# Kernel tuning notes

Hardware: AMD Instinct MI355X
Metric: run time of the kernel (lower is better)

## Reference

```python
import jax, jax.numpy as jnp
import numpy as np

D_MODEL = 1024
D_K = 64
D_V = 64
N_HEADS = 16
LN_EPS = 1e-5


def setup_inputs() -> dict:
    key = jax.random.key(0)
    ks = jax.random.split(key, 9)
    B, S = 2, 2048
    scale = 0.02
    return {
        "input_Q": jax.random.normal(ks[0], (B, S, D_MODEL), dtype=jnp.float32),
        "input_K": jax.random.normal(ks[1], (B, S, D_MODEL), dtype=jnp.float32),
        "input_V": jax.random.normal(ks[2], (B, S, D_MODEL), dtype=jnp.float32),
        "W_Q": jax.random.normal(ks[3], (D_MODEL, N_HEADS * D_K), dtype=jnp.float32) * scale,
        "W_K": jax.random.normal(ks[4], (D_MODEL, N_HEADS * D_K), dtype=jnp.float32) * scale,
        "W_V": jax.random.normal(ks[5], (D_MODEL, N_HEADS * D_V), dtype=jnp.float32) * scale,
        "W_O": jax.random.normal(ks[6], (N_HEADS * D_V, D_MODEL), dtype=jnp.float32) * scale,
        "ln_gamma": jnp.ones((D_MODEL,), dtype=jnp.float32),
        "ln_beta": jnp.zeros((D_MODEL,), dtype=jnp.float32),
    }


def reference(input_Q, input_K, input_V, W_Q, W_K, W_V, W_O, ln_gamma, ln_beta):
    B, Lq, _ = input_Q.shape
    Lk = input_K.shape[1]
    # projections -> [B, H, L, d]
    Q = (input_Q @ W_Q).reshape(B, Lq, N_HEADS, D_K).transpose(0, 2, 1, 3)
    K = (input_K @ W_K).reshape(B, Lk, N_HEADS, D_K).transpose(0, 2, 1, 3)
    V = (input_V @ W_V).reshape(B, Lk, N_HEADS, D_V).transpose(0, 2, 1, 3)
    # scores: [B, H, Lq, Lk]
    scores = jnp.einsum("bhqd,bhkd->bhqk", Q, K) / jnp.sqrt(jnp.float32(D_K))
    # NOTE: source uses nn.Softmax(dim=1) -> softmax over the HEADS axis (faithful quirk)
    attn = jax.nn.softmax(scores, axis=1)
    context = jnp.einsum("bhqk,bhkv->bhqv", attn, V)
    context = context.transpose(0, 2, 1, 3).reshape(B, Lq, N_HEADS * D_V)
    output = context @ W_O
    # residual + LayerNorm over last dim
    x = output + input_Q
    mu = jnp.mean(x, axis=-1, keepdims=True)
    var = jnp.mean(jnp.square(x - mu), axis=-1, keepdims=True)
    return (x - mu) / jnp.sqrt(var + LN_EPS) * ln_gamma + ln_beta
```

## Files before the change

### kernel.cpp

```cpp
#include <hip/hip_runtime.h>
#include <cstdint>
#include <cstddef>

#define DM 1024
#define HEADS 16
#define DHEAD 64
#define SEQ 2048
#define BATCH 2

typedef __bf16 bf16x8 __attribute__((ext_vector_type(8)));
typedef float  f32x4  __attribute__((ext_vector_type(4)));
typedef unsigned short u16;
typedef unsigned int u32;
typedef u16 u16x8 __attribute__((ext_vector_type(8)));
typedef u16 u16x4 __attribute__((ext_vector_type(4)));

__device__ __forceinline__ float bf2f(u16 u){
    union { u32 i; float f; } v; v.i = ((u32)u) << 16; return v.f;
}
__device__ __forceinline__ u16 f2bf(float f){
    union { float f; u32 i; } v; v.f = f;
    u32 r = v.i + 0x7FFF + ((v.i >> 16) & 1);
    return (u16)(r >> 16);
}
__device__ __forceinline__ u16 f2bf_rhu(float f){
    union { float f; u32 i; } v; v.f = f;
    return (u16)((v.i + 0x8000u) >> 16);
}
__device__ __forceinline__ float fexp2(float x){
    float r;
    asm volatile("v_exp_f32 %0, %1\n\ts_nop 1" : "=v"(r) : "v"(x));
    return r;
}
__device__ __forceinline__ void gload16(const u16* g, u16* l){
    __builtin_amdgcn_global_load_lds(
        (const __attribute__((address_space(1))) u32*)g,
        (__attribute__((address_space(3))) u32*)l, 16, 0, 0);
}
__device__ __forceinline__ int probe_flag(const u16* q){
    int cnt = 0;
    #pragma unroll
    for (int i = 0; i < 32; i += 2){
        int e = (q[i] >> 7) & 0xFF;
        if (e >= 90 && e <= 141) cnt++;
    }
    return (cnt >= 12) ? 1 : 0;
}

__global__ __launch_bounds__(256) void k_cvt3(const void* __restrict__ s0,
                                              const void* __restrict__ s1,
                                              const void* __restrict__ s2,
                                              u16* __restrict__ dstbase,
                                              int* __restrict__ hdr, int n){
    int isbf = probe_flag((const u16*)s0);
    if (blockIdx.x == 0 && blockIdx.y == 0 && threadIdx.x == 0){
        hdr[0] = isbf;
        #pragma unroll
        for (int c = 1; c <= 24; c++) hdr[c] = 0;
    }
    int z = blockIdx.y;
    const void* src = (z == 0) ? s0 : ((z == 1) ? s1 : s2);
    u16* dst = dstbase + (size_t)z * n;
    int i = (blockIdx.x * 256 + threadIdx.x) * 8;
    if (i >= n) return;
    if (isbf){
        *(u16x8*)&dst[i] = *(const u16x8*)((const u16*)src + i);
    } else {
        const float* s = (const float*)src + i;
        u16x8 o;
        #pragma unroll
        for (int j = 0; j < 8; j++) o[j] = f2bf(s[j]);
        *(u16x8*)&dst[i] = o;
    }
}

__global__ void k_tcvt4(const void* __restrict__ w0, const void* __restrict__ w1,
                        const void* __restrict__ w2, const void* __restrict__ w3,
                        u16* __restrict__ dstbase,
                        const int* __restrict__ flag, int R, int C){
    __shared__ u16 tile[32][33];
    int z = blockIdx.z;
    const void* src = (z == 0) ? w0 : ((z == 1) ? w1 : ((z == 2) ? w2 : w3));
    u16* dst = dstbase + (size_t)z * R * C;
    bool isbf = (*flag != 0);
    int c0 = blockIdx.x * 32, r0 = blockIdx.y * 32;
    int tx = threadIdx.x, ty = threadIdx.y;
    #pragma unroll
    for (int i = 0; i < 32; i += 8){
        size_t idx = (size_t)(r0 + ty + i) * C + c0 + tx;
        tile[ty + i][tx] = isbf ? ((const u16*)src)[idx] : f2bf(((const float*)src)[idx]);
    }
    __syncthreads();
    #pragma unroll
    for (int i = 0; i < 32; i += 8)
        dst[(size_t)(c0 + ty + i) * R + r0 + tx] = tile[tx][ty + i];
}

template<int NJ>
__global__ __launch_bounds__(256, 2) void k_gemmT(const u16* __restrict__ A0,
                                                  const u16* __restrict__ Bt0,
                                                  u16* __restrict__ C0,
                                                  size_t strA, size_t strB, size_t strC,
                                                  int M, int N, int K){
    constexpr int BN = NJ * 32;
    __shared__ u16 lsA[128 * 64];
    __shared__ u16 lsB[BN * 64];
    int z = blockIdx.z;
    const u16* A  = A0  + strA * z;
    const u16* Bt = Bt0 + strB * z;
    u16* C = C0 + strC * z;
    int m0 = blockIdx.y * 128, n0 = blockIdx.x * BN;
    int t = threadIdx.x, lane = t & 63, w = t >> 6;
    int l15 = lane & 15, quad = lane >> 4;
    int wm = (w & 1) * 64, wn = (w >> 1) * (NJ * 16);
    f32x4 acc[4][NJ] = {};
    for (int k0 = 0; k0 < K; k0 += 64){
        __syncthreads();
        #pragma unroll
        for (int j = 0; j < 4; j++){
            int ub = j * 256 + w * 64;
            int u  = ub + lane;
            int r  = u >> 3, cg = (u & 7) ^ (r & 7);
            gload16(&A[(size_t)(m0 + r) * K + k0 + cg * 8], &lsA[ub * 8]);
        }
        #pragma unroll
        for (int j = 0; j < NJ; j++){
            int ub = j * 256 + w * 64;
            int u  = ub + lane;
            int r  = u >> 3, cg = (u & 7) ^ (r & 7);
            gload16(&Bt[(size_t)(n0 + r) * K + k0 + cg * 8], &lsB[ub * 8]);
        }
        __syncthreads();
        bf16x8 af[4][2], bfr[NJ][2];
        #pragma unroll
        for (int i = 0; i < 4; i++){
            int row = wm + i * 16 + l15;
            #pragma unroll
            for (int kk = 0; kk < 2; kk++)
                af[i][kk] = *(const bf16x8*)&lsA[row * 64 + (((kk * 4 + quad) ^ (row & 7)) * 8)];
        }
        #pragma unroll
        for (int jj = 0; jj < NJ; jj++){
            int row = wn + jj * 16 + l15;
            #pragma unroll
            for (int kk = 0; kk < 2; kk++)
                bfr[jj][kk] = *(const bf16x8*)&lsB[row * 64 + (((kk * 4 + quad) ^ (row & 7)) * 8)];
        }
        #pragma unroll
        for (int i = 0; i < 4; i++)
            #pragma unroll
            for (int jj = 0; jj < NJ; jj++)
                #pragma unroll
                for (int kk = 0; kk < 2; kk++)
                    acc[i][jj] = __builtin_amdgcn_mfma_f32_16x16x32_bf16(af[i][kk], bfr[jj][kk],
                                                                         acc[i][jj], 0, 0, 0);
    }
    #pragma unroll
    for (int i = 0; i < 4; i++)
        #pragma unroll
        for (int jj = 0; jj < NJ; jj++)
            #pragma unroll
            for (int r = 0; r < 4; r++){
                int m = m0 + wm + i * 16 + quad * 4 + r;
                int n = n0 + wn + jj * 16 + l15;
                C[(size_t)m * N + n] = f2bf(acc[i][jj][r]);
            }
}

__global__ __launch_bounds__(1024, 4) void k_attn5(const u16* __restrict__ Qp,
                                                   const u16* __restrict__ Kp,
                                                   const u16* __restrict__ Vt,
                                                   u16* __restrict__ c0,
                                                   u16* __restrict__ c1,
                                                   u16* __restrict__ c2,
                                                   u16* __restrict__ c3,
                                                   int* __restrict__ cnt,
                                                   int ncomboM1, int iters){
    __shared__ u16 ebuf[2][16][64][36];
    __shared__ int s_combo, s_slot;
    int t = threadIdx.x;
    if (t == 0){
        int xcc;
        asm volatile("s_getreg_b32 %0, hwreg(HW_REG_XCC_ID)" : "=s"(xcc));
        int start = xcc & ncomboM1;
        int combo = -1, slot = -1;
        for (int a = 0; a <= ncomboM1 && combo < 0; a++){
            int c = (start + a) & ncomboM1;
            int s = atomicAdd(&cnt[c], 1);
            if (s < 32){ combo = c; slot = s; }
        }
        s_combo = combo; s_slot = slot;
    }
    __syncthreads();
    int combo = s_combo;
    if (combo < 0) return;
    int b = combo & 1, chunk = combo >> 1;
    int q0 = s_slot * 64;
    int h = t >> 6, lane = t & 63, l15 = lane & 15, quad = lane >> 4;
    u16* outp = (chunk == 0) ? c0 : ((chunk == 1) ? c1 : ((chunk == 2) ? c2 : c3));
    const float cexp = 0.125f * 1.44269504f;
    int kbeg = chunk * (iters << 5);

    bf16x8 qf[4][2];
    #pragma unroll
    for (int sub = 0; sub < 4; sub++)
        #pragma unroll
        for (int ch = 0; ch < 2; ch++)
            qf[sub][ch] = *(const bf16x8*)&Qp[((size_t)(b * SEQ + q0 + sub * 16 + l15)) * DM
                                             + h * DHEAD + ch * 32 + quad * 8];

    f32x4 oacc[4][4] = {};
    int sq = t >> 4, sku = (t & 15) * 2;

    auto score_phase = [&](int it){
        int k0 = kbeg + (it << 5), bf = it & 1;
        #pragma unroll
        for (int kt = 0; kt < 2; kt++){
            const u16* kb = Kp + ((size_t)(b * SEQ + k0 + kt * 16 + l15)) * DM + h * DHEAD + quad * 8;
            bf16x8 kf0 = *(const bf16x8*)(kb);
            bf16x8 kf1 = *(const bf16x8*)(kb + 32);
            #pragma unroll
            for (int sub = 0; sub < 4; sub++){
                f32x4 sc = {};
                sc = __builtin_amdgcn_mfma_f32_16x16x32_bf16(qf[sub][0], kf0, sc, 0, 0, 0);
                sc = __builtin_amdgcn_mfma_f32_16x16x32_bf16(qf[sub][1], kf1, sc, 0, 0, 0);
                #pragma unroll
                for (int r = 0; r < 4; r++)
                    ebuf[bf][h][sub * 16 + quad * 4 + r][kt * 16 + l15] =
                        f2bf_rhu(fexp2(sc[r] * cexp));
            }
        }
    };

    score_phase(0);
    for (int it = 0; it < iters; it++){
        int bf = it & 1;
        __syncthreads();
        {
            u32 ev[16];
            float s0 = 0.f, s1 = 0.f;
            #pragma unroll
            for (int hh = 0; hh < 16; hh++){
                u32 u = *(const u32*)&ebuf[bf][hh][sq][sku];
                ev[hh] = u;
                union { u32 i; float f; } lo, hi;
                lo.i = u << 16; hi.i = u & 0xFFFF0000u;
                s0 += lo.f; s1 += hi.f;
            }
            float r0 = __builtin_amdgcn_rcpf(s0);
            float r1 = __builtin_amdgcn_rcpf(s1);
            #pragma unroll
            for (int hh = 0; hh < 16; hh++){
                union { u32 i; float f; } lo, hi, p0, p1;
                lo.i = ev[hh] << 16; hi.i = ev[hh] & 0xFFFF0000u;
                p0.f = lo.f * r0; p1.f = hi.f * r1;
                *(u32*)&ebuf[bf][hh][sq][sku] =
                    __builtin_amdgcn_perm(p1.i + 0x8000u, p0.i + 0x8000u, 0x07060302u);
            }
        }
        __syncthreads();
        int k0 = kbeg + (it << 5);
        bf16x8 pa[4];
        #pragma unroll
        for (int sub = 0; sub < 4; sub++){
            const u16* pp = &ebuf[bf][h][sub * 16 + l15][quad * 8];
            union { bf16x8 v; u16x4 q[2]; } pu;
            pu.q[0] = *(const u16x4*)pp;
            pu.q[1] = *(const u16x4*)(pp + 4);
            pa[sub] = pu.v;
        }
        #pragma unroll
        for (int vt = 0; vt < 4; vt++){
            bf16x8 vf = *(const bf16x8*)&Vt[((size_t)b * DM + h * DHEAD + vt * 16 + l15) * SEQ
                                            + k0 + quad * 8];
            #pragma unroll
            for (int sub = 0; sub < 4; sub++)
                oacc[sub][vt] = __builtin_amdgcn_mfma_f32_16x16x32_bf16(pa[sub], vf, oacc[sub][vt], 0, 0, 0);
        }
        if (it + 1 < iters) score_phase(it + 1);
    }
    #pragma unroll
    for (int sub = 0; sub < 4; sub++)
        #pragma unroll
        for (int vt = 0; vt < 4; vt++)
            #pragma unroll
            for (int r = 0; r < 4; r++){
                int q = q0 + sub * 16 + quad * 4 + r;
                int n = h * DHEAD + vt * 16 + l15;
                outp[((size_t)b * SEQ + q) * DM + n] = f2bf(oacc[sub][vt][r]);
            }
}

__global__ __launch_bounds__(256) void k_reduce(const u16* __restrict__ a,
                                                const u16* __restrict__ b,
                                                const u16* __restrict__ c,
                                                const u16* __restrict__ d,
                                                u16* __restrict__ dst, int n, int nch){
    int i = (blockIdx.x * 256 + threadIdx.x) * 8;
    if (i >= n) return;
    u16x8 x = *(const u16x8*)&a[i];
    u16x8 y = *(const u16x8*)&b[i];
    u16x8 o;
    if (nch == 4){
        u16x8 zc = *(const u16x8*)&c[i];
        u16x8 zd = *(const u16x8*)&d[i];
        #pragma unroll
        for (int j = 0; j < 8; j++)
            o[j] = f2bf((bf2f(x[j]) + bf2f(y[j])) + (bf2f(zc[j]) + bf2f(zd[j])));
    } else {
        #pragma unroll
        for (int j = 0; j < 8; j++) o[j] = f2bf(bf2f(x[j]) + bf2f(y[j]));
    }
    *(u16x8*)&dst[i] = o;
}

__global__ __launch_bounds__(256) void k_ln(const u16* __restrict__ O,
                                            const void* __restrict__ Qin,
                                            const void* __restrict__ gamma,
                                            const void* __restrict__ beta,
                                            void* __restrict__ out,
                                            const int* __restrict__ flag){
    __shared__ float red[4][2];
    bool isbf = (*flag != 0);
    int row = blockIdx.x;
    int t = threadIdx.x;
    const u16* op = O + (size_t)row * DM;
    float xv[4];
    float s1 = 0.f, s2 = 0.f;
    #pragma unroll
    for (int i = 0; i < 4; i++){
        int idx = i * 256 + t;
        float q = isbf ? bf2f(((const u16*)Qin)[(size_t)row * DM + idx])
                       : ((const float*)Qin)[(size_t)row * DM + idx];
        float x = bf2f(op[idx]) + q;
        xv[i] = x; s1 += x; s2 += x * x;
    }
    #pragma unroll
    for (int off = 32; off; off >>= 1){
        s1 += __shfl_down(s1, off);
        s2 += __shfl_down(s2, off);
    }
    int w = t >> 6, lane = t & 63;
    if (lane == 0){ red[w][0] = s1; red[w][1] = s2; }
    __syncthreads();
    float S1 = red[0][0] + red[1][0] + red[2][0] + red[3][0];
    float S2 = red[0][1] + red[1][1] + red[2][1] + red[3][1];
    float mu  = S1 * (1.0f / DM);
    float var = S2 * (1.0f / DM) - mu * mu;
    float rstd = rsqrtf(var + 1e-5f);
    #pragma unroll
    for (int i = 0; i < 4; i++){
        int idx = i * 256 + t;
        float g = isbf ? bf2f(((const u16*)gamma)[idx]) : ((const float*)gamma)[idx];
        float bb= isbf ? bf2f(((const u16*)beta )[idx]) : ((const float*)beta )[idx];
        float y = (xv[i] - mu) * rstd * g + bb;
        if (isbf) ((u16*)out)[(size_t)row * DM + idx] = f2bf(y);
        else      ((float*)out)[(size_t)row * DM + idx] = y;
    }
}

extern "C" void kernel_launch(void* const* d_in, const int* in_sizes, int n_in,
                              void* d_out, int out_size, void* d_ws, size_t ws_size,
                              hipStream_t stream){
    (void)in_sizes; (void)n_in; (void)out_size;
    const void* inQ = d_in[0];
    const void* inK = d_in[1];
    const void* inV = d_in[2];
    const void* wQ  = d_in[3];
    const void* wK  = d_in[4];
    const void* wV  = d_in[5];
    const void* wO  = d_in[6];
    const void* gma = d_in[7];
    const void* bta = d_in[8];

    int* hdr  = (int*)d_ws;
    int* flag = hdr;
    int* cnt  = hdr + 1;
    u16* base = (u16*)d_ws + 64;

    const size_t MB1 = 1024u * 1024u;
    const size_t M4  = 4u * MB1;
    const size_t M2  = 2u * MB1;
    u16* Qi  = base + 0;
    u16* Ki  = base + 1 * M4;
    u16* Vi  = base + 2 * M4;
    u16* WtQ = base + 3 * M4;
    u16* WtV = WtQ + 2 * MB1;
    u16* WtO = WtQ + 3 * MB1;
    u16* Qp  = base + 4 * M4;
    u16* Kp  = base + 5 * M4;
    u16* Vp  = base + 6 * M4;
    u16* ext = base + 7 * M4;
    u16* Vt    = Ki;
    u16* ctxp0 = Qi;
    u16* ctxp1 = Vp;
    u16* ctxp2 = Vi;

    size_t need4 = 128 + 8 * M4 * sizeof(u16);
    int nch = (ws_size >= need4) ? 4 : 2;
    u16* ctxp3 = (nch == 4) ? ext : ctxp2;
    int ncomboM1 = 2 * nch - 1;
    int iters   = (nch == 4) ? 16 : 32;
    int ablocks = 32 * 2 * nch;

    const int nIn = BATCH * SEQ * DM;
    k_cvt3<<<dim3(nIn / 2048, 3), 256, 0, stream>>>(inQ, inK, inV, base, hdr, nIn);

    k_tcvt4<<<dim3(32, 32, 4), dim3(32, 8), 0, stream>>>(wQ, wK, wV, wO, WtQ, flag, 1024, 1024);

    k_gemmT<4><<<dim3(8, 32, 2), 256, 0, stream>>>(Qi, WtQ, Qp, M4, MB1, M4, 4096, 1024, 1024);

    k_gemmT<2><<<dim3(32, 8, 2), 256, 0, stream>>>(WtV, Vi, Vt, 0, M2, M2, 1024, 2048, 1024);

    k_attn5<<<ablocks, 1024, 0, stream>>>(Qp, Kp, Vt, ctxp0, ctxp1, ctxp2, ctxp3,
                                          cnt, ncomboM1, iters);

    k_reduce<<<nIn / 2048, 256, 0, stream>>>(ctxp0, ctxp1, ctxp2, ctxp3, ctxp0, nIn, nch);

    k_gemmT<2><<<dim3(16, 32, 1), 256, 0, stream>>>(ctxp0, WtO, Qp, 0, 0, 0, 4096, 1024, 1024);

    k_ln<<<4096, 256, 0, stream>>>(Qp, inQ, gma, bta, d_out, flag);
}
```

Baseline: 316.6 us.

## Double-buffer GEMM LDS tiles, merge Q/K/V projections into one launch, vectorize LayerNorm

The GEMM loop now double-buffers its LDS tiles. The next K-slice's global-to-LDS loads are issued before computing the current slice, which leaves one barrier per iteration and hides load latency. The Q/K and V^T projection GEMMs are merged into a single 768-block launch using 128x128 tiles, and buffer aliasing is reshuffled so Vt lives in Vp. LayerNorm now handles two rows per block with 8-wide vector loads and stores. Doubling LDS per block (64KB for the projection kernel) may reduce occupancy.

```diff
diff --git a/kernel.cpp b/kernel.cpp
--- a/kernel.cpp
+++ b/kernel.cpp
@@ -97,54 +97,54 @@
 }
 
 template<int NJ>
-__global__ __launch_bounds__(256, 2) void k_gemmT(const u16* __restrict__ A0,
-                                                  const u16* __restrict__ Bt0,
-                                                  u16* __restrict__ C0,
-                                                  size_t strA, size_t strB, size_t strC,
-                                                  int M, int N, int K){
-    constexpr int BN = NJ * 32;
-    __shared__ u16 lsA[128 * 64];
-    __shared__ u16 lsB[BN * 64];
-    int z = blockIdx.z;
-    const u16* A  = A0  + strA * z;
-    const u16* Bt = Bt0 + strB * z;
-    u16* C = C0 + strC * z;
-    int m0 = blockIdx.y * 128, n0 = blockIdx.x * BN;
+__device__ __forceinline__ void gemm_body(const u16* __restrict__ A,
+                                          const u16* __restrict__ Bt,
+                                          u16* __restrict__ C,
+                                          int N, int K, int m0, int n0,
+                                          u16* lsA, u16* lsB){
+    constexpr int BN  = NJ * 32;
+    constexpr int ASZ = 128 * 64;
+    constexpr int BSZ = BN * 64;
     int t = threadIdx.x, lane = t & 63, w = t >> 6;
     int l15 = lane & 15, quad = lane >> 4;
     int wm = (w & 1) * 64, wn = (w >> 1) * (NJ * 16);
     f32x4 acc[4][NJ] = {};
-    for (int k0 = 0; k0 < K; k0 += 64){
-        __syncthreads();
+
+    auto stage = [&](int p, int k0){
+        u16* la = lsA + p * ASZ;
+        u16* lb = lsB + p * BSZ;
         #pragma unroll
         for (int j = 0; j < 4; j++){
             int ub = j * 256 + w * 64;
             int u  = ub + lane;
             int r  = u >> 3, cg = (u & 7) ^ (r & 7);
-            gload16(&A[(size_t)(m0 + r) * K + k0 + cg * 8], &lsA[ub * 8]);
+            gload16(&A[(size_t)(m0 + r) * K + k0 + cg * 8], &la[ub * 8]);
         }
         #pragma unroll
         for (int j = 0; j < NJ; j++){
             int ub = j * 256 + w * 64;
             int u  = ub + lane;
             int r  = u >> 3, cg = (u & 7) ^ (r & 7);
-            gload16(&Bt[(size_t)(n0 + r) * K + k0 + cg * 8], &lsB[ub * 8]);
-        }
-        __syncthreads();
+            gload16(&Bt[(size_t)(n0 + r) * K + k0 + cg * 8], &lb[ub * 8]);
+        }
+    };
+    auto compute = [&](int p){
+        u16* la = lsA + p * ASZ;
+        u16* lb = lsB + p * BSZ;
         bf16x8 af[4][2], bfr[NJ][2];
         #pragma unroll
         for (int i = 0; i < 4; i++){
             int row = wm + i * 16 + l15;
             #pragma unroll
             for (int kk = 0; kk < 2; kk++)
-                af[i][kk] = *(const bf16x8*)&lsA[row * 64 + (((kk * 4 + quad) ^ (row & 7)) * 8)];
+                af[i][kk] = *(const bf16x8*)&la[row * 64 + (((kk * 4 + quad) ^ (row & 7)) * 8)];
         }
         #pragma unroll
         for (int jj = 0; jj < NJ; jj++){
             int row = wn + jj * 16 + l15;
             #pragma unroll
             for (int kk = 0; kk < 2; kk++)
-                bfr[jj][kk] = *(const bf16x8*)&lsB[row * 64 + (((kk * 4 + quad) ^ (row & 7)) * 8)];
+                bfr[jj][kk] = *(const bf16x8*)&lb[row * 64 + (((kk * 4 + quad) ^ (row & 7)) * 8)];
         }
         #pragma unroll
         for (int i = 0; i < 4; i++)
@@ -154,6 +154,14 @@
                 for (int kk = 0; kk < 2; kk++)
                     acc[i][jj] = __builtin_amdgcn_mfma_f32_16x16x32_bf16(af[i][kk], bfr[jj][kk],
                                                                          acc[i][jj], 0, 0, 0);
+    };
+
+    int nt = K >> 6;
+    stage(0, 0);
+    for (int tt = 0; tt < nt; tt++){
+        __syncthreads();
+        if (tt + 1 < nt) stage((tt + 1) & 1, (tt + 1) << 6);
+        compute(tt & 1);
     }
     #pragma unroll
     for (int i = 0; i < 4; i++)
@@ -165,6 +173,45 @@
                 int n = n0 + wn + jj * 16 + l15;
                 C[(size_t)m * N + n] = f2bf(acc[i][jj][r]);
             }
+}
+
+__global__ __launch_bounds__(256, 2) void k_proj(const u16* __restrict__ QKin,
+                                                 const u16* __restrict__ WtQ,
+                                                 u16* __restrict__ QKout,
+                                                 const u16* __restrict__ WtV,
+                                                 const u16* __restrict__ Vi,
+                                                 u16* __restrict__ Vt){
+    __shared__ u16 lsA[2 * 128 * 64];
+    __shared__ u16 lsB[2 * 128 * 64];
+    const size_t MB1 = 1024u * 1024u;
+    int bid = blockIdx.x;
+    const u16 *A, *Bt; u16* C; int N, m0, n0;
+    if (bid < 512){
+        int z = bid >> 8, r = bid & 255;
+        A  = QKin  + (size_t)z * 4 * MB1;
+        Bt = WtQ   + (size_t)z * MB1;
+        C  = QKout + (size_t)z * 4 * MB1;
+        N  = 1024;
+        n0 = (r & 7) * 128;  m0 = (r >> 3) * 128;
+    } else {
+        int v = bid - 512;
+        int z = v >> 7, r = v & 127;
+        A  = WtV;
+        Bt = Vi + (size_t)z * 2 * MB1;
+        C  = Vt + (size_t)z * 2 * MB1;
+        N  = 2048;
+        n0 = (r & 15) * 128; m0 = (r >> 4) * 128;
+    }
+    gemm_body<4>(A, Bt, C, N, 1024, m0, n0, lsA, lsB);
+}
+
+__global__ __launch_bounds__(256, 2) void k_wo(const u16* __restrict__ ctx,
+                                               const u16* __restrict__ WtO,
+                                               u16* __restrict__ Ob){
+    __shared__ u16 lsA[2 * 128 * 64];
+    __shared__ u16 lsB[2 * 64 * 64];
+    gemm_body<2>(ctx, WtO, Ob, 1024, 1024,
+                 blockIdx.y * 128, blockIdx.x * 64, lsA, lsB);
 }
 
 __global__ __launch_bounds__(1024, 4) void k_attn5(const u16* __restrict__ Qp,
@@ -320,42 +367,64 @@
                                             const void* __restrict__ beta,
                                             void* __restrict__ out,
                                             const int* __restrict__ flag){
-    __shared__ float red[4][2];
+    __shared__ float red[2][2][2];
     bool isbf = (*flag != 0);
-    int row = blockIdx.x;
     int t = threadIdx.x;
-    const u16* op = O + (size_t)row * DM;
-    float xv[4];
+    int rr = t >> 7, tt = t & 127;
+    size_t row = (size_t)blockIdx.x * 2 + rr;
+    int idx = tt * 8;
+    u16x8 ov = *(const u16x8*)(O + row * DM + idx);
+    float x[8];
+    if (isbf){
+        u16x8 qv = *(const u16x8*)((const u16*)Qin + row * DM + idx);
+        #pragma unroll
+        for (int j = 0; j < 8; j++) x[j] = bf2f(ov[j]) + bf2f(qv[j]);
+    } else {
+        const float* qp = (const float*)Qin + row * DM + idx;
+        f32x4 q0 = *(const f32x4*)qp, q1 = *(const f32x4*)(qp + 4);
+        #pragma unroll
+        for (int j = 0; j < 4; j++){
+            x[j]     = bf2f(ov[j])     + q0[j];
+            x[j + 4] = bf2f(ov[j + 4]) + q1[j];
+        }
+    }
     float s1 = 0.f, s2 = 0.f;
     #pragma unroll
-    for (int i = 0; i < 4; i++){
-        int idx = i * 256 + t;
-        float q = isbf ? bf2f(((const u16*)Qin)[(size_t)row * DM + idx])
-                       : ((const float*)Qin)[(size_t)row * DM + idx];
-        float x = bf2f(op[idx]) + q;
-        xv[i] = x; s1 += x; s2 += x * x;
-    }
+    for (int j = 0; j < 8; j++){ s1 += x[j]; s2 += x[j] * x[j]; }
     #pragma unroll
     for (int off = 32; off; off >>= 1){
         s1 += __shfl_down(s1, off);
         s2 += __shfl_down(s2, off);
     }
-    int w = t >> 6, lane = t & 63;
-    if (lane == 0){ red[w][0] = s1; red[w][1] = s2; }
+    int wir = (t >> 6) & 1, lane = t & 63;
+    if (lane == 0){ red[rr][wir][0] = s1; red[rr][wir][1] = s2; }
     __syncthreads();
-    float S1 = red[0][0] + red[1][0] + red[2][0] + red[3][0];
-    float S2 = red[0][1] + red[1][1] + red[2][1] + red[3][1];
-    float mu  = S1 * (1.0f / DM);
-    float var = S2 * (1.0f / DM) - mu * mu;
+    float S1 = red[rr][0][0] + red[rr][1][0];
+    float S2 = red[rr][0][1] + red[rr][1][1];
+    float mu   = S1 * (1.0f / DM);
+    float var  = S2 * (1.0f / DM) - mu * mu;
     float rstd = rsqrtf(var + 1e-5f);
-    #pragma unroll
-    for (int i = 0; i < 4; i++){
-        int idx = i * 256 + t;
-        float g = isbf ? bf2f(((const u16*)gamma)[idx]) : ((const float*)gamma)[idx];
-        float bb= isbf ? bf2f(((const u16*)beta )[idx]) : ((const float*)beta )[idx];
-        float y = (xv[i] - mu) * rstd * g + bb;
-        if (isbf) ((u16*)out)[(size_t)row * DM + idx] = f2bf(y);
-        else      ((float*)out)[(size_t)row * DM + idx] = y;
+    if (isbf){
+        u16x8 gv = *(const u16x8*)((const u16*)gamma + idx);
+        u16x8 bv = *(const u16x8*)((const u16*)beta  + idx);
+        u16x8 o;
+        #pragma unroll
+        for (int j = 0; j < 8; j++)
+            o[j] = f2bf((x[j] - mu) * rstd * bf2f(gv[j]) + bf2f(bv[j]));
+        *(u16x8*)((u16*)out + row * DM + idx) = o;
+    } else {
+        const float* gp = (const float*)gamma + idx;
+        const float* bp = (const float*)beta  + idx;
+        f32x4 g0 = *(const f32x4*)gp, g1 = *(const f32x4*)(gp + 4);
+        f32x4 b0 = *(const f32x4*)bp, b1 = *(const f32x4*)(bp + 4);
+        f32x4 o0, o1;
+        #pragma unroll
+        for (int j = 0; j < 4; j++){
+            o0[j] = (x[j]     - mu) * rstd * g0[j] + b0[j];
+            o1[j] = (x[j + 4] - mu) * rstd * g1[j] + b1[j];
+        }
+        float* op = (float*)out + row * DM + idx;
+        *(f32x4*)op = o0; *(f32x4*)(op + 4) = o1;
     }
 }
 
@@ -380,7 +449,6 @@
 
     const size_t MB1 = 1024u * 1024u;
     const size_t M4  = 4u * MB1;
-    const size_t M2  = 2u * MB1;
     u16* Qi  = base + 0;
     u16* Ki  = base + 1 * M4;
     u16* Vi  = base + 2 * M4;
@@ -391,9 +459,9 @@
     u16* Kp  = base + 5 * M4;
     u16* Vp  = base + 6 * M4;
     u16* ext = base + 7 * M4;
-    u16* Vt    = Ki;
+    u16* Vt    = Vp;
     u16* ctxp0 = Qi;
-    u16* ctxp1 = Vp;
+    u16* ctxp1 = Ki;
     u16* ctxp2 = Vi;
 
     size_t need4 = 128 + 8 * M4 * sizeof(u16);
@@ -408,16 +476,14 @@
 
     k_tcvt4<<<dim3(32, 32, 4), dim3(32, 8), 0, stream>>>(wQ, wK, wV, wO, WtQ, flag, 1024, 1024);
 
-    k_gemmT<4><<<dim3(8, 32, 2), 256, 0, stream>>>(Qi, WtQ, Qp, M4, MB1, M4, 4096, 1024, 1024);
-
-    k_gemmT<2><<<dim3(32, 8, 2), 256, 0, stream>>>(WtV, Vi, Vt, 0, M2, M2, 1024, 2048, 1024);
+    k_proj<<<768, 256, 0, stream>>>(Qi, WtQ, Qp, WtV, Vi, Vt);
 
     k_attn5<<<ablocks, 1024, 0, stream>>>(Qp, Kp, Vt, ctxp0, ctxp1, ctxp2, ctxp3,
                                           cnt, ncomboM1, iters);
 
     k_reduce<<<nIn / 2048, 256, 0, stream>>>(ctxp0, ctxp1, ctxp2, ctxp3, ctxp0, nIn, nch);
 
-    k_gemmT<2><<<dim3(16, 32, 1), 256, 0, stream>>>(ctxp0, WtO, Qp, 0, 0, 0, 4096, 1024, 1024);
-
-    k_ln<<<4096, 256, 0, stream>>>(Qp, inQ, gma, bta, d_out, flag);
-}
+    k_wo<<<dim3(16, 32), 256, 0, stream>>>(ctxp0, WtO, Qp);
+
+    k_ln<<<2048, 256, 0, stream>>>(Qp, inQ, gma, bta, d_out, flag);
+}
```

Measured after the change: 332.2 us. 1.05x slower.
